# Performance work log

Measured on AMD Instinct MI355X. Metric: run time of the kernel, lower is better.

Reference implementation:

```python
import jax, jax.numpy as jnp
import numpy as np

B, L, D = 2, 2048, 1024
H, E = 16, 64  # n_heads, per-head dim (E_q=E_k=E_v)
EPS = 1e-5


def _layernorm(x):
    # fresh nn.LayerNorm each forward: gamma=1, beta=0, eps=1e-5 (biased var)
    mu = jnp.mean(x, axis=-1, keepdims=True)
    var = jnp.mean(jnp.square(x - mu), axis=-1, keepdims=True)
    return (x - mu) * jax.lax.rsqrt(var + EPS)


def setup_inputs() -> dict:
    key = jax.random.key(0)
    ks = jax.random.split(key, 9)
    s_in = 1.0 / np.sqrt(D)
    s_ctx = 1.0 / np.sqrt(H * E)
    return {
        "query": jax.random.normal(ks[0], (B, L, D), jnp.float32),
        "key": jax.random.normal(ks[1], (B, L, D), jnp.float32),
        "value": jax.random.normal(ks[2], (B, L, D), jnp.float32),
        # torch nn.Linear weights are [out_features, in_features]
        "W_Q": jax.random.uniform(ks[3], (H * E, D), jnp.float32, -s_in, s_in),
        "W_K": jax.random.uniform(ks[4], (H * E, D), jnp.float32, -s_in, s_in),
        "W_V": jax.random.uniform(ks[5], (H * E, D), jnp.float32, -s_in, s_in),
        "W_O": jax.random.uniform(ks[6], (D, H * E), jnp.float32, -s_ctx, s_ctx),
        "fc_w": jax.random.uniform(ks[7], (D, D), jnp.float32, -s_in, s_in),
        "fc_b": jax.random.uniform(ks[8], (D,), jnp.float32, -s_in, s_in),
    }


def reference(query, key, value, W_Q, W_K, W_V, W_O, fc_w, fc_b):
    b = query.shape[0]
    # projections -> [B, H, L, E]
    q = (query @ W_Q.T).reshape(b, -1, H, E).transpose(0, 2, 1, 3)
    k = (key @ W_K.T).reshape(b, -1, H, E).transpose(0, 2, 1, 3)
    v = (value @ W_V.T).reshape(b, -1, H, E).transpose(0, 2, 1, 3)
    scores = jnp.einsum('bhqe,bhke->bhqk', q, k) / np.sqrt(E).astype(np.float32)
    A = jax.nn.softmax(scores, axis=-1)                 # [B,H,Lq,Lk]
    ctx = jnp.einsum('bhqk,bhke->bhqe', A, v)           # [B,H,L,E]
    ctx = ctx.transpose(0, 2, 1, 3).reshape(b, -1, H * E)
    attn_out = ctx @ W_O.T                               # dropout = identity (eval)
    x = _layernorm(attn_out + query)
    out = x @ fc_w.T + fc_b                              # dropout = identity (eval)
    out = _layernorm(x + out)
    return out
```

## Files before the change

### kernel.cpp

```cpp
#include <hip/hip_runtime.h>
#include <stdint.h>

typedef unsigned short u16;
typedef __bf16 bf16x8 __attribute__((ext_vector_type(8)));
typedef __bf16 bf16x4 __attribute__((ext_vector_type(4)));
typedef float f32x4 __attribute__((ext_vector_type(4)));

#define MFMA16(a,b,c) __builtin_amdgcn_mfma_f32_16x16x32_bf16((a),(b),(c),0,0,0)

__device__ __forceinline__ bf16x4 pack4(float a, float b, float c, float d){
  bf16x4 r; r[0]=(__bf16)a; r[1]=(__bf16)b; r[2]=(__bf16)c; r[3]=(__bf16)d; return r;
}

__device__ __forceinline__ void gl2lds16(const void* g, void* l){
  __builtin_amdgcn_global_load_lds(
      (const __attribute__((address_space(1))) unsigned int*)g,
      (__attribute__((address_space(3))) unsigned int*)l, 16, 0, 0);
}

__device__ __forceinline__ bf16x8 ldsfrag(const u16* base, int row, int gr){
  return *(const bf16x8*)(base + row * 64 + ((gr ^ (row & 7)) << 3));
}

template<int NB, int BN>
__device__ __forceinline__ void gemm_core(const u16* __restrict__ A,
                                          const u16* __restrict__ Bt,
                                          int N, int K, int mode,
                                          void* __restrict__ Cout,
                                          const float* __restrict__ bias,
                                          float oscale)
{
  constexpr int NF = BN / 32;
  __shared__ u16 Al[NB][128 * 64];
  __shared__ u16 Bl[NB][BN * 64];
  const int tid  = threadIdx.x;
  const int lane = tid & 63;
  const int w    = tid >> 6;
  const int wr   = w >> 1, wc = w & 1;
  const int l15  = lane & 15, g = lane >> 4;
  const int rowBase = blockIdx.y << 7;
  const int colBase = blockIdx.x * BN;

  const int srow = tid >> 3;
  const int swz  = ((tid & 7) ^ (srow & 7)) << 3;
  const u16* Ag = A  + (size_t)(rowBase + srow) * K + swz;
  const u16* Bg = Bt + (size_t)(colBase + srow) * K + swz;

  f32x4 acc[4][NF];
#pragma unroll
  for (int m = 0; m < 4; ++m)
#pragma unroll
    for (int n = 0; n < NF; ++n) acc[m][n] = f32x4{0.f, 0.f, 0.f, 0.f};

  auto stage = [&](int buf, int k0) {
#pragma unroll
    for (int i = 0; i < 4; ++i)
      gl2lds16(Ag + (size_t)(i * 32) * K + k0, Al[buf] + i * 2048 + w * 512);
#pragma unroll
    for (int i = 0; i < BN / 32; ++i)
      gl2lds16(Bg + (size_t)(i * 32) * K + k0, Bl[buf] + i * 2048 + w * 512);
  };
  auto compute = [&](int buf) {
    __builtin_amdgcn_s_setprio(1);
#pragma unroll
    for (int kk = 0; kk < 2; ++kk) {
      bf16x8 af[4], bfr[NF];
#pragma unroll
      for (int m = 0; m < 4; ++m) af[m]  = ldsfrag(Al[buf], wr * 64 + m * 16 + l15, kk * 4 + g);
#pragma unroll
      for (int n = 0; n < NF; ++n) bfr[n] = ldsfrag(Bl[buf], wc * (BN/2) + n * 16 + l15, kk * 4 + g);
#pragma unroll
      for (int m = 0; m < 4; ++m)
#pragma unroll
        for (int n = 0; n < NF; ++n)
          acc[m][n] = MFMA16(af[m], bfr[n], acc[m][n]);
    }
    __builtin_amdgcn_s_setprio(0);
  };

  if (NB == 2) {
    stage(0, 0);
    __syncthreads();
    int cur = 0;
    for (int k0 = 0; k0 < K; k0 += 64) {
      if (k0 + 64 < K) stage(cur ^ 1, k0 + 64);
      compute(cur);
      __syncthreads();
      cur ^= 1;
    }
  } else {
    for (int k0 = 0; k0 < K; k0 += 64) {
      stage(0, k0);
      __syncthreads();
      compute(0);
      __syncthreads();
    }
  }

#pragma unroll
  for (int m = 0; m < 4; ++m) {
#pragma unroll
    for (int n = 0; n < NF; ++n) {
      const int row0 = rowBase + wr * 64 + m * 16 + g * 4;
      const int col  = colBase + wc * (BN/2) + n * 16 + l15;
      if (mode == 1) {
        const int b = row0 >> 11, l = row0 & 2047;
        const int h = col >> 6,  e = col & 63;
        *(bf16x4*)((u16*)Cout + ((size_t)((((b << 4) + h) << 6) | e) << 11) + l) =
            pack4(acc[m][n][0], acc[m][n][1], acc[m][n][2], acc[m][n][3]);
      } else {
        const float bb = (mode == 4) ? bias[col] : 0.f;
#pragma unroll
        for (int r = 0; r < 4; ++r) {
          const int row = row0 + r;
          const float v = acc[m][n][r];
          if (mode == 0) {
            *(__bf16*)((u16*)Cout + (size_t)row * N + col) = (__bf16)(v * oscale);
          } else {
            *(__bf16*)((u16*)Cout + (size_t)row * N + col) = (__bf16)(v + bb);
          }
        }
      }
    }
  }
}

#define QSCALE 0.18033688011112042f

__global__ __launch_bounds__(256) void k_proj(
    const u16* __restrict__ qb, const u16* __restrict__ kb, const u16* __restrict__ vb,
    const u16* __restrict__ wq, const u16* __restrict__ wk, const u16* __restrict__ wv,
    u16* __restrict__ Qp, u16* __restrict__ Kp, u16* __restrict__ Vt)
{
  const int z = blockIdx.z;
  const u16* A = (z == 0) ? qb : (z == 1) ? kb : vb;
  const u16* B = (z == 0) ? wq : (z == 1) ? wk : wv;
  void* C = (z == 0) ? (void*)Qp : (z == 1) ? (void*)Kp : (void*)Vt;
  gemm_core<2, 64>(A, B, 1024, 1024, (z == 2) ? 1 : 0, C, nullptr, (z == 0) ? QSCALE : 1.0f);
}

__global__ __launch_bounds__(256) void k_gemm_o(const u16* __restrict__ A,
                                                const u16* __restrict__ B,
                                                u16* __restrict__ C)
{ gemm_core<2, 64>(A, B, 1024, 1024, 0, (void*)C, nullptr, 1.0f); }

__global__ __launch_bounds__(256) void k_gemm_fc(const u16* __restrict__ A,
                                                 const u16* __restrict__ B,
                                                 u16* __restrict__ C,
                                                 const float* __restrict__ bias)
{ gemm_core<2, 64>(A, B, 1024, 1024, 4, (void*)C, bias, 1.0f); }

__global__ __launch_bounds__(256, 2) void k_attn(const u16* __restrict__ Qp,
                                                 const u16* __restrict__ Kp,
                                                 const u16* __restrict__ Vt,
                                                 float* __restrict__ Opart,
                                                 float* __restrict__ dpart)
{
  __shared__ u16 Klds[2][64 * 64];
  __shared__ u16 Vlds[2][64 * 64];
  __shared__ u16 Plds[4][32 * 64];

  const int tid = threadIdx.x, lane = tid & 63, w = tid >> 6;
  const int l15 = lane & 15, g = lane >> 4, l7 = l15 & 7;
  const int bh = blockIdx.y, b = bh >> 4, h = bh & 15;
  const int q0 = blockIdx.x << 7;
  const int half = blockIdx.z;
  const int kvbase = half << 10;

  bf16x8 bq[2][2];
#pragma unroll
  for (int u = 0; u < 2; ++u) {
    const u16* Qr = Qp + (((size_t)((b << 11) + q0 + (w << 5) + (u << 4) + l15)) << 10)
                  + (h << 6) + (g << 3);
    bq[u][0] = *(const bf16x8*)(Qr);
    bq[u][1] = *(const bf16x8*)(Qr + 32);
  }

  const f32x4 zero4 = {0.f, 0.f, 0.f, 0.f};
  f32x4 o0[4], o1[4];
#pragma unroll
  for (int f = 0; f < 4; ++f) { o0[f] = zero4; o1[f] = zero4; }
  float ds0 = 0.f, ds1 = 0.f;

  const int srow = tid >> 3;
  const int swz  = ((tid & 7) ^ (srow & 7)) << 3;
  const u16* Kg = Kp + (((size_t)((b << 11) + kvbase + srow)) << 10) + (h << 6) + swz;
  const u16* Vg = Vt + (((size_t)((bh << 6) + srow)) << 11) + kvbase + swz;
  u16* Pw = Plds[w];

  auto stage = [&](int buf, int j0) {
#pragma unroll
    for (int i = 0; i < 2; ++i) {
      gl2lds16(Kg + ((size_t)(j0 + i * 32) << 10), Klds[buf] + i * 2048 + w * 512);
      gl2lds16(Vg + ((size_t)(i * 32) << 11) + j0, Vlds[buf] + i * 2048 + w * 512);
    }
  };

  stage(0, 0);
  __syncthreads();
  int cur = 0;

  for (int j0 = 0; j0 < 1024; j0 += 64) {
    if (j0 + 64 < 1024) stage(cur ^ 1, j0 + 64);

    bf16x8 kf[4][2];
#pragma unroll
    for (int f = 0; f < 4; ++f) {
      kf[f][0] = ldsfrag(Klds[cur], f * 16 + l15, g);
      kf[f][1] = ldsfrag(Klds[cur], f * 16 + l15, 4 + g);
    }
    f32x4 s0[4], s1[4];
    __builtin_amdgcn_s_setprio(1);
#pragma unroll
    for (int f = 0; f < 4; ++f) {
      s0[f] = MFMA16(kf[f][0], bq[0][0], zero4);
      s0[f] = MFMA16(kf[f][1], bq[0][1], s0[f]);
      s1[f] = MFMA16(kf[f][0], bq[1][0], zero4);
      s1[f] = MFMA16(kf[f][1], bq[1][1], s1[f]);
    }
    __builtin_amdgcn_s_setprio(0);

#pragma unroll
    for (int f = 0; f < 4; ++f) {
      const float a0 = __builtin_amdgcn_exp2f(s0[f][0]);
      const float a1 = __builtin_amdgcn_exp2f(s0[f][1]);
      const float a2 = __builtin_amdgcn_exp2f(s0[f][2]);
      const float a3 = __builtin_amdgcn_exp2f(s0[f][3]);
      ds0 += (a0 + a1) + (a2 + a3);
      *(bf16x4*)(Pw + l15 * 64 + ((((2 * f) + (g >> 1)) ^ l7) << 3) + ((g & 1) << 2)) =
          pack4(a0, a1, a2, a3);
      const float c0 = __builtin_amdgcn_exp2f(s1[f][0]);
      const float c1 = __builtin_amdgcn_exp2f(s1[f][1]);
      const float c2 = __builtin_amdgcn_exp2f(s1[f][2]);
      const float c3 = __builtin_amdgcn_exp2f(s1[f][3]);
      ds1 += (c0 + c1) + (c2 + c3);
      *(bf16x4*)(Pw + (16 + l15) * 64 + ((((2 * f) + (g >> 1)) ^ l7) << 3) + ((g & 1) << 2)) =
          pack4(c0, c1, c2, c3);
    }
    asm volatile("s_waitcnt lgkmcnt(0)" ::: "memory");
    __builtin_amdgcn_sched_barrier(0);

    bf16x8 vf[4][2];
#pragma unroll
    for (int f = 0; f < 4; ++f) {
      vf[f][0] = ldsfrag(Vlds[cur], f * 16 + l15, g);
      vf[f][1] = ldsfrag(Vlds[cur], f * 16 + l15, 4 + g);
    }
    __builtin_amdgcn_s_setprio(1);
#pragma unroll
    for (int kk = 0; kk < 2; ++kk) {
      const bf16x8 pb0 = *(const bf16x8*)(Pw + l15 * 64 + (((kk * 4 + g) ^ l7) << 3));
      const bf16x8 pb1 = *(const bf16x8*)(Pw + (16 + l15) * 64 + (((kk * 4 + g) ^ l7) << 3));
#pragma unroll
      for (int f = 0; f < 4; ++f) {
        o0[f] = MFMA16(vf[f][kk], pb0, o0[f]);
        o1[f] = MFMA16(vf[f][kk], pb1, o1[f]);
      }
    }
    __builtin_amdgcn_s_setprio(0);
    __syncthreads();
    cur ^= 1;
  }

  ds0 += __shfl_xor(ds0, 16, 64);
  ds0 += __shfl_xor(ds0, 32, 64);
  ds1 += __shfl_xor(ds1, 16, 64);
  ds1 += __shfl_xor(ds1, 32, 64);

  const int brow0 = (b << 11) + q0 + (w << 5) + l15;
  const int brow1 = brow0 + 16;
  float* Op = Opart + ((size_t)half << 22);
#pragma unroll
  for (int f = 0; f < 4; ++f) {
    *(f32x4*)(Op + ((size_t)brow0 << 10) + (h << 6) + f * 16 + (g << 2)) = o0[f];
    *(f32x4*)(Op + ((size_t)brow1 << 10) + (h << 6) + f * 16 + (g << 2)) = o1[f];
  }
  if (g == 0) {
    dpart[(half << 16) + (brow0 << 4) + h] = ds0;
    dpart[(half << 16) + (brow1 << 4) + h] = ds1;
  }
}

__global__ __launch_bounds__(256) void k_combine(const float* __restrict__ Opart,
                                                 const float* __restrict__ dpart,
                                                 u16* __restrict__ ctx)
{
  const int row = blockIdx.x, tid = threadIdx.x;
  const int h = tid >> 4;
  const float d = dpart[(row << 4) + h] + dpart[(1 << 16) + (row << 4) + h];
  const float inv = 1.0f / d;
  const f32x4 p0 = ((const f32x4*)(Opart + ((size_t)row << 10)))[tid];
  const f32x4 p1 = ((const f32x4*)(Opart + (1u << 22) + ((size_t)row << 10)))[tid];
  ((bf16x4*)(ctx + ((size_t)row << 10)))[tid] =
      pack4((p0[0] + p1[0]) * inv, (p0[1] + p1[1]) * inv,
            (p0[2] + p1[2]) * inv, (p0[3] + p1[3]) * inv);
}

__device__ __forceinline__ void ln_stats(float4 t, int tid, float& mean, float& inv){
  float s = t.x + t.y + t.z + t.w;
  float q = t.x * t.x + t.y * t.y + t.z * t.z + t.w * t.w;
#pragma unroll
  for (int d = 1; d < 64; d <<= 1) {
    s += __shfl_xor(s, d, 64);
    q += __shfl_xor(q, d, 64);
  }
  __shared__ float ps[4], pq[4];
  const int w = tid >> 6;
  if ((tid & 63) == 0) { ps[w] = s; pq[w] = q; }
  __syncthreads();
  s = ps[0] + ps[1] + ps[2] + ps[3];
  q = pq[0] + pq[1] + pq[2] + pq[3];
  mean = s * (1.0f / 1024.0f);
  const float var = q * (1.0f / 1024.0f) - mean * mean;
  inv = rsqrtf(var + 1e-5f);
}

__global__ __launch_bounds__(256) void k_ln1(const u16* __restrict__ a,
                                             const float* __restrict__ res,
                                             u16* __restrict__ xb)
{
  const int row = blockIdx.x, tid = threadIdx.x;
  const size_t base = (size_t)row << 10;
  const bf16x4 av = ((const bf16x4*)(a + base))[tid];
  const float4 rr = ((const float4*)(res + base))[tid];
  float4 t;
  t.x = (float)av[0] + rr.x; t.y = (float)av[1] + rr.y;
  t.z = (float)av[2] + rr.z; t.w = (float)av[3] + rr.w;
  float mean, inv;
  ln_stats(t, tid, mean, inv);
  ((bf16x4*)(xb + base))[tid] = pack4((t.x - mean) * inv, (t.y - mean) * inv,
                                      (t.z - mean) * inv, (t.w - mean) * inv);
}

__global__ __launch_bounds__(256) void k_ln2(const u16* __restrict__ a,
                                             const u16* __restrict__ res,
                                             float* __restrict__ out)
{
  const int row = blockIdx.x, tid = threadIdx.x;
  const size_t base = (size_t)row << 10;
  const bf16x4 av = ((const bf16x4*)(a + base))[tid];
  const bf16x4 rv = ((const bf16x4*)(res + base))[tid];
  float4 t;
  t.x = (float)av[0] + (float)rv[0]; t.y = (float)av[1] + (float)rv[1];
  t.z = (float)av[2] + (float)rv[2]; t.w = (float)av[3] + (float)rv[3];
  float mean, inv;
  ln_stats(t, tid, mean, inv);
  float4 o;
  o.x = (t.x - mean) * inv; o.y = (t.y - mean) * inv;
  o.z = (t.z - mean) * inv; o.w = (t.w - mean) * inv;
  ((float4*)(out + base))[tid] = o;
}

__global__ __launch_bounds__(256) void k_cvt3(const float* __restrict__ q,
                                              const float* __restrict__ k,
                                              const float* __restrict__ v,
                                              u16* __restrict__ qo,
                                              u16* __restrict__ ko,
                                              u16* __restrict__ vo)
{
  const int z = blockIdx.y;
  const float* src = (z == 0) ? q : (z == 1) ? k : v;
  u16* dst = (z == 0) ? qo : (z == 1) ? ko : vo;
  const int i = blockIdx.x * 256 + threadIdx.x;
  const float4 t = ((const float4*)src)[i];
  ((bf16x4*)dst)[i] = pack4(t.x, t.y, t.z, t.w);
}

__global__ __launch_bounds__(256) void k_cvt5(const float* __restrict__ a0,
                                              const float* __restrict__ a1,
                                              const float* __restrict__ a2,
                                              const float* __restrict__ a3,
                                              const float* __restrict__ a4,
                                              u16* __restrict__ o0, u16* __restrict__ o1,
                                              u16* __restrict__ o2, u16* __restrict__ o3,
                                              u16* __restrict__ o4)
{
  const int z = blockIdx.y;
  const float* src = (z == 0) ? a0 : (z == 1) ? a1 : (z == 2) ? a2 : (z == 3) ? a3 : a4;
  u16* dst = (z == 0) ? o0 : (z == 1) ? o1 : (z == 2) ? o2 : (z == 3) ? o3 : o4;
  const int i = blockIdx.x * 256 + threadIdx.x;
  const float4 t = ((const float4*)src)[i];
  ((bf16x4*)dst)[i] = pack4(t.x, t.y, t.z, t.w);
}

extern "C" void kernel_launch(void* const* d_in, const int* in_sizes, int n_in,
                              void* d_out, int out_size, void* d_ws, size_t ws_size,
                              hipStream_t stream)
{
  (void)in_sizes; (void)n_in; (void)out_size; (void)ws_size;
  const float* query = (const float*)d_in[0];
  const float* key   = (const float*)d_in[1];
  const float* value = (const float*)d_in[2];
  const float* W_Q   = (const float*)d_in[3];
  const float* W_K   = (const float*)d_in[4];
  const float* W_V   = (const float*)d_in[5];
  const float* W_O   = (const float*)d_in[6];
  const float* fc_w  = (const float*)d_in[7];
  const float* fc_b  = (const float*)d_in[8];
  float* out = (float*)d_out;
  char* ws = (char*)d_ws;

  u16*   qb    = (u16*)(ws + 0);
  u16*   kb    = (u16*)(ws + 8388608);
  u16*   vb    = (u16*)(ws + 16777216);
  u16*   wq    = (u16*)(ws + 25165824);
  u16*   wk    = (u16*)(ws + 27262976);
  u16*   wv    = (u16*)(ws + 29360128);
  u16*   wo    = (u16*)(ws + 31457280);
  u16*   fw    = (u16*)(ws + 33554432);
  u16*   Qp    = (u16*)(ws + 35651584);
  u16*   Kp    = (u16*)(ws + 44040192);
  u16*   Vt    = (u16*)(ws + 52428800);
  u16*   ctx   = (u16*)(ws + 60817408);
  float* Opart = (float*)(ws + 69206016);
  float* dpart = (float*)(ws + 102760448);
  u16*   attnb = (u16*)(ws + 69206016);
  u16*   xb    = vb;
  u16*   yb    = qb;

  k_cvt3<<<dim3(4096, 3), 256, 0, stream>>>(query, key, value, qb, kb, vb);
  k_cvt5<<<dim3(1024, 5), 256, 0, stream>>>(W_Q, W_K, W_V, W_O, fc_w, wq, wk, wv, wo, fw);
  k_proj<<<dim3(16, 32, 3), 256, 0, stream>>>(qb, kb, vb, wq, wk, wv, Qp, Kp, Vt);
  k_attn<<<dim3(16, 32, 2), 256, 0, stream>>>(Qp, Kp, Vt, Opart, dpart);
  k_combine<<<dim3(4096), 256, 0, stream>>>(Opart, dpart, ctx);
  k_gemm_o<<<dim3(16, 32), 256, 0, stream>>>(ctx, wo, attnb);
  k_ln1<<<dim3(4096), 256, 0, stream>>>(attnb, query, xb);
  k_gemm_fc<<<dim3(16, 32), 256, 0, stream>>>(xb, fw, yb, fc_b);
  k_ln2<<<dim3(4096), 256, 0, stream>>>(yb, xb, out);
}
```

Before: 164.4 us.

## Keep softmax probabilities in registers and use K=16 MFMA for PV

The attention kernel no longer writes P tiles to LDS and reads them back. The bf16 probabilities stay in registers in the S-accumulator layout and feed 16x16x16 MFMAs directly, with V fragments loaded as 4-element pieces to match. This removes the P shared-memory round trip and its waitcnt barrier, and frees LDS so launch bounds can request 4 blocks per CU. The cost is twice as many smaller MFMA instructions and more, narrower V LDS reads, plus possible register pressure under the tighter occupancy bound.

```diff
diff --git a/kernel.cpp b/kernel.cpp
--- a/kernel.cpp
+++ b/kernel.cpp
@@ -4,9 +4,24 @@
 typedef unsigned short u16;
 typedef __bf16 bf16x8 __attribute__((ext_vector_type(8)));
 typedef __bf16 bf16x4 __attribute__((ext_vector_type(4)));
+typedef short s16x4 __attribute__((ext_vector_type(4)));
 typedef float f32x4 __attribute__((ext_vector_type(4)));
 
 #define MFMA16(a,b,c) __builtin_amdgcn_mfma_f32_16x16x32_bf16((a),(b),(c),0,0,0)
+
+__device__ __forceinline__ f32x4 mfma_k16(bf16x4 a, bf16x4 b, f32x4 c){
+#if __has_builtin(__builtin_amdgcn_mfma_f32_16x16x16_bf16)
+  return __builtin_amdgcn_mfma_f32_16x16x16_bf16(a, b, c, 0, 0, 0);
+#elif __has_builtin(__builtin_amdgcn_mfma_f32_16x16x16bf16_1k)
+  s16x4 ai, bi;
+  __builtin_memcpy(&ai, &a, 8);
+  __builtin_memcpy(&bi, &b, 8);
+  return __builtin_amdgcn_mfma_f32_16x16x16bf16_1k(ai, bi, c, 0, 0, 0);
+#else
+  asm("v_mfma_f32_16x16x16_bf16 %0, %1, %2, %0" : "+v"(c) : "v"(a), "v"(b));
+  return c;
+#endif
+}
 
 __device__ __forceinline__ bf16x4 pack4(float a, float b, float c, float d){
   bf16x4 r; r[0]=(__bf16)a; r[1]=(__bf16)b; r[2]=(__bf16)c; r[3]=(__bf16)d; return r;
@@ -20,6 +35,9 @@
 
 __device__ __forceinline__ bf16x8 ldsfrag(const u16* base, int row, int gr){
   return *(const bf16x8*)(base + row * 64 + ((gr ^ (row & 7)) << 3));
+}
+__device__ __forceinline__ bf16x4 ldsfrag64(const u16* base, int row, int gr, int h){
+  return *(const bf16x4*)(base + row * 64 + ((gr ^ (row & 7)) << 3) + (h << 2));
 }
 
 template<int NB, int BN>
@@ -150,7 +168,7 @@
                                                  const float* __restrict__ bias)
 { gemm_core<2, 64>(A, B, 1024, 1024, 4, (void*)C, bias, 1.0f); }
 
-__global__ __launch_bounds__(256, 2) void k_attn(const u16* __restrict__ Qp,
+__global__ __launch_bounds__(256, 4) void k_attn(const u16* __restrict__ Qp,
                                                  const u16* __restrict__ Kp,
                                                  const u16* __restrict__ Vt,
                                                  float* __restrict__ Opart,
@@ -158,10 +176,9 @@
 {
   __shared__ u16 Klds[2][64 * 64];
   __shared__ u16 Vlds[2][64 * 64];
-  __shared__ u16 Plds[4][32 * 64];
 
   const int tid = threadIdx.x, lane = tid & 63, w = tid >> 6;
-  const int l15 = lane & 15, g = lane >> 4, l7 = l15 & 7;
+  const int l15 = lane & 15, g = lane >> 4;
   const int bh = blockIdx.y, b = bh >> 4, h = bh & 15;
   const int q0 = blockIdx.x << 7;
   const int half = blockIdx.z;
@@ -186,7 +203,6 @@
   const int swz  = ((tid & 7) ^ (srow & 7)) << 3;
   const u16* Kg = Kp + (((size_t)((b << 11) + kvbase + srow)) << 10) + (h << 6) + swz;
   const u16* Vg = Vt + (((size_t)((bh << 6) + srow)) << 11) + kvbase + swz;
-  u16* Pw = Plds[w];
 
   auto stage = [&](int buf, int j0) {
 #pragma unroll
@@ -203,23 +219,20 @@
   for (int j0 = 0; j0 < 1024; j0 += 64) {
     if (j0 + 64 < 1024) stage(cur ^ 1, j0 + 64);
 
-    bf16x8 kf[4][2];
-#pragma unroll
-    for (int f = 0; f < 4; ++f) {
-      kf[f][0] = ldsfrag(Klds[cur], f * 16 + l15, g);
-      kf[f][1] = ldsfrag(Klds[cur], f * 16 + l15, 4 + g);
-    }
     f32x4 s0[4], s1[4];
     __builtin_amdgcn_s_setprio(1);
 #pragma unroll
     for (int f = 0; f < 4; ++f) {
-      s0[f] = MFMA16(kf[f][0], bq[0][0], zero4);
-      s0[f] = MFMA16(kf[f][1], bq[0][1], s0[f]);
-      s1[f] = MFMA16(kf[f][0], bq[1][0], zero4);
-      s1[f] = MFMA16(kf[f][1], bq[1][1], s1[f]);
+      const bf16x8 ka = ldsfrag(Klds[cur], f * 16 + l15, g);
+      const bf16x8 kb = ldsfrag(Klds[cur], f * 16 + l15, 4 + g);
+      s0[f] = MFMA16(ka, bq[0][0], zero4);
+      s0[f] = MFMA16(kb, bq[0][1], s0[f]);
+      s1[f] = MFMA16(ka, bq[1][0], zero4);
+      s1[f] = MFMA16(kb, bq[1][1], s1[f]);
     }
     __builtin_amdgcn_s_setprio(0);
 
+    bf16x4 p0[4], p1[4];
 #pragma unroll
     for (int f = 0; f < 4; ++f) {
       const float a0 = __builtin_amdgcn_exp2f(s0[f][0]);
@@ -227,34 +240,23 @@
       const float a2 = __builtin_amdgcn_exp2f(s0[f][2]);
       const float a3 = __builtin_amdgcn_exp2f(s0[f][3]);
       ds0 += (a0 + a1) + (a2 + a3);
-      *(bf16x4*)(Pw + l15 * 64 + ((((2 * f) + (g >> 1)) ^ l7) << 3) + ((g & 1) << 2)) =
-          pack4(a0, a1, a2, a3);
+      p0[f] = pack4(a0, a1, a2, a3);
       const float c0 = __builtin_amdgcn_exp2f(s1[f][0]);
       const float c1 = __builtin_amdgcn_exp2f(s1[f][1]);
       const float c2 = __builtin_amdgcn_exp2f(s1[f][2]);
       const float c3 = __builtin_amdgcn_exp2f(s1[f][3]);
       ds1 += (c0 + c1) + (c2 + c3);
-      *(bf16x4*)(Pw + (16 + l15) * 64 + ((((2 * f) + (g >> 1)) ^ l7) << 3) + ((g & 1) << 2)) =
-          pack4(c0, c1, c2, c3);
-    }
-    asm volatile("s_waitcnt lgkmcnt(0)" ::: "memory");
-    __builtin_amdgcn_sched_barrier(0);
-
-    bf16x8 vf[4][2];
-#pragma unroll
-    for (int f = 0; f < 4; ++f) {
-      vf[f][0] = ldsfrag(Vlds[cur], f * 16 + l15, g);
-      vf[f][1] = ldsfrag(Vlds[cur], f * 16 + l15, 4 + g);
-    }
+      p1[f] = pack4(c0, c1, c2, c3);
+    }
+
     __builtin_amdgcn_s_setprio(1);
 #pragma unroll
-    for (int kk = 0; kk < 2; ++kk) {
-      const bf16x8 pb0 = *(const bf16x8*)(Pw + l15 * 64 + (((kk * 4 + g) ^ l7) << 3));
-      const bf16x8 pb1 = *(const bf16x8*)(Pw + (16 + l15) * 64 + (((kk * 4 + g) ^ l7) << 3));
+    for (int fe = 0; fe < 4; ++fe) {
 #pragma unroll
       for (int f = 0; f < 4; ++f) {
-        o0[f] = MFMA16(vf[f][kk], pb0, o0[f]);
-        o1[f] = MFMA16(vf[f][kk], pb1, o1[f]);
+        const bf16x4 va = ldsfrag64(Vlds[cur], fe * 16 + l15, 2 * f + (g >> 1), g & 1);
+        o0[fe] = mfma_k16(va, p0[f], o0[fe]);
+        o1[fe] = mfma_k16(va, p1[f], o1[fe]);
       }
     }
     __builtin_amdgcn_s_setprio(0);
```

Result: faster. 159.1 us (-3.2%).
